# Kernel optimization log

Measured on AMD Instinct MI355X. Metric: run time of the kernel, lower is better.

Reference implementation:

```python
import jax, jax.numpy as jnp
import numpy as np

N_TH1 = 30
LB = 1e-20
UB = 1e20
LB_EXP = -20.0
UB_EXP = 20.0


def make_directions(n_th1):
    # Reproduces the TF __init__ direction sampling on the sphere.
    n_th2 = 2 * (n_th1 - 1) + 1
    th1 = np.linspace(-np.pi / 2, np.pi / 2, n_th1)
    th2 = np.linspace(-np.pi, np.pi, n_th2)
    c1, s1 = np.cos(th1), np.sin(th1)
    c2, s2 = np.cos(th2), np.sin(th2)
    dx = np.outer(c1[1:-1], c2[:-1])          # [n_th1-2, n_th2-1]
    dy = np.outer(c1[1:-1], s2[:-1])
    dz = np.broadcast_to(s1[1:-1, None], dx.shape)
    mid = np.stack([dx, dy, dz], -1).reshape(-1, 3)
    poles = np.array([[c1[0] * c2[0], c1[0] * s2[0], s1[0]],
                      [c1[-1] * c2[0], c1[-1] * s2[0], s1[-1]]])
    return np.concatenate([mid, poles], 0).astype(np.float32)  # [D, 3]


def setup_inputs() -> dict:
    key = jax.random.key(0)
    k1, k2, k3 = jax.random.split(key, 3)
    vertices = jax.random.normal(k1, (8, 64, 32, 3), jnp.float32)
    # smoothness is a p-norm exponent; realistic range [2, 20]
    smoothness = 2.0 + 18.0 * jax.random.uniform(k2, (8, 64), jnp.float32)
    pointcloud = jax.random.normal(k3, (8, 2048, 3), jnp.float32)
    return {"vertices": vertices, "smoothness": smoothness, "pointcloud": pointcloud}


def _spt_forward(vertices, smoothness):
    dirs = jnp.asarray(make_directions(N_TH1))            # [D, 3]
    B, P = vertices.shape[0], vertices.shape[1]
    mean_v = jnp.mean(vertices, axis=2, keepdims=True)    # [B,P,1,3]
    local_v = vertices - mean_v                           # [B,P,V,3]

    # z = <v, x> for every vertex/direction pair -> [B,P,V,D]
    z = jnp.einsum('bpvc,dc->bpvd', local_v, dirs)
    zm = jnp.maximum(z, 0.0)
    p = smoothness[:, :, None, None]                      # [B,P,1,1]

    # dynamic rescaling k = 10^ceil(...) to keep zm^p in fp range
    zm_max = jnp.max(zm, axis=2, keepdims=True)           # [B,P,1,D]
    zm_log = jnp.log(zm_max) / jnp.log(10.0)              # = max over V of log10(zm)
    exponent = zm_log * p
    lk = jnp.where(exponent < LB_EXP, (-15.0 - exponent) / p, 0.0)
    k = 10.0 ** jnp.clip(jnp.ceil(lk), 0.0, UB_EXP)       # [B,P,1,D]
    k = jax.lax.stop_gradient(k)                          # ceil has zero grad anyway

    zm = zm * k
    pos = zm > 0
    # clip(zm^p, lb, ub) - (zm==0)*lb  ==  where(zm>0, clip(zm^p,lb,ub), 0)
    zm_p = jnp.where(pos, jnp.clip(jnp.where(pos, zm, 1.0) ** p, LB, UB), 0.0)
    sum_zm_p = jnp.sum(zm_p, axis=2, keepdims=True)       # [B,P,1,D]
    spos = sum_zm_p > 0
    h = jnp.where(spos, jnp.clip(jnp.where(spos, sum_zm_p, 1.0) ** (1.0 / p), LB, UB), LB)

    # dh/dz = clip((zm/h)^(p-1), lb, ub)
    ratio = zm / h                                        # [B,P,V,D]
    rpos = ratio > 0
    dhdz = jnp.where(rpos, jnp.clip(jnp.where(rpos, ratio, 1.0) ** (p - 1.0), LB, UB), LB)
    # dh/dx = dhdz^T @ vertices -> surface points
    dhdx = jnp.einsum('bpvd,bpvc->bpdc', dhdz, local_v)   # [B,P,D,3]
    surf = dhdx + mean_v                                  # broadcast [B,P,1,3]

    h_out = jnp.clip(h / k, -UB, UB)                      # [B,P,1,D]
    h_out = jnp.transpose(h_out, (0, 1, 3, 2))            # [B,P,D,1]
    local_dirs = jnp.broadcast_to(dirs[None, None], (B, P) + dirs.shape)
    direction_h = jnp.concatenate([local_dirs, h_out], axis=-1)  # [B,P,D,4]
    points = surf.reshape(B, -1, 3)                       # [B, P*D, 3]
    mean_out = mean_v.reshape(B, P, 3)
    return points, direction_h, mean_out, local_v


def reference(vertices, smoothness, pointcloud):
    points, direction_h, mean_out, local_v = _spt_forward(vertices, smoothness)
    B, P = vertices.shape[0], vertices.shape[1]
    # overlap / retraction loops are truncated in the source; placeholders
    overlap = jnp.zeros((B, P, 1), jnp.float32)
    retraction = jnp.zeros((B, P, 1), jnp.float32)
    return (points, direction_h, overlap, retraction, mean_out, local_v)
```

## Files before the change

kernel.cpp:

```cpp
#include <hip/hip_runtime.h>
#include <math.h>

#define NBP 512
#define VV 32
#define DD 1626
#define DHALF 813

#define O_POINTS 0
#define O_DIRH   2497536
#define O_OVER   5827584
#define O_RETR   5828096
#define O_MEAN   5828608
#define O_LOCAL  5830144

#define L10_2 0.3010299956639812f
#define L2_10 3.321928094887362f
#define LH_MIN -66.43856189774725f

__device__ __forceinline__ float fexp2(float x) {
  return __builtin_amdgcn_exp2f(x);
}

__device__ __forceinline__ void make_dir_fast(int d, float& x, float& y, float& z) {
  if (d < 1624) {
    const int i1 = d / 58 + 1;
    const int i2 = d - (i1 - 1) * 58;
    const float STEP = 0.10833078115826873f;
    const float th1 = -1.5707963267948966f + (float)i1 * STEP;
    const float th2 = -3.14159265358979323846f + (float)i2 * STEP;
    const float s1 = __sinf(th1);
    const float c1 = __cosf(th1);
    const float s2 = __sinf(th2);
    const float c2 = __cosf(th2);
    x = c1 * c2; y = c1 * s2; z = s1;
  } else if (d == 1624) {
    x = -6.123234e-17f; y = -7.49880e-33f; z = -1.0f;
  } else {
    x = -6.123234e-17f; y = -7.49880e-33f; z = 1.0f;
  }
}

__global__ __launch_bounds__(256) void spt_kernel(
    const float* __restrict__ vertices,
    const float* __restrict__ smooth,
    float* __restrict__ out)
{
  const int bp   = blockIdx.x;
  const int half = blockIdx.y;
  const int tid  = threadIdx.x;

  const int dbase = half * DHALF;

  float t[VV * 3];
  {
    const float4* vp4 = (const float4*)(vertices + bp * (VV * 3));
#pragma unroll
    for (int j = 0; j < 24; j++) {
      float4 q = vp4[j];
      t[j * 4 + 0] = q.x; t[j * 4 + 1] = q.y;
      t[j * 4 + 2] = q.z; t[j * 4 + 3] = q.w;
    }
  }

  float mxa = 0.f, mxb = 0.f, mya = 0.f, myb = 0.f, mza = 0.f, mzb = 0.f;
#pragma unroll
  for (int i = 0; i < VV; i += 2) {
    mxa += t[3 * i + 0];  mxb += t[3 * i + 3];
    mya += t[3 * i + 1];  myb += t[3 * i + 4];
    mza += t[3 * i + 2];  mzb += t[3 * i + 5];
  }
  const float mx = (mxa + mxb) * (1.0f / 32.0f);
  const float my = (mya + myb) * (1.0f / 32.0f);
  const float mz = (mza + mzb) * (1.0f / 32.0f);

#pragma unroll
  for (int i = 0; i < VV; i++) {
    t[3 * i + 0] -= mx;
    t[3 * i + 1] -= my;
    t[3 * i + 2] -= mz;
  }

  if (half == 1 && tid == 0) {
    float4* lp = (float4*)(out + O_LOCAL + bp * (VV * 3));
#pragma unroll
    for (int j = 0; j < 24; j++) {
      lp[j] = make_float4(t[j * 4 + 0], t[j * 4 + 1], t[j * 4 + 2], t[j * 4 + 3]);
    }
    out[O_MEAN + bp * 3 + 0] = mx;
    out[O_MEAN + bp * 3 + 1] = my;
    out[O_MEAN + bp * 3 + 2] = mz;
    out[O_OVER + bp] = 0.f;
    out[O_RETR + bp] = 0.f;
  }

  const float p     = smooth[bp];
  const float inv_p = 1.0f / p;
  const float pm1   = p - 1.0f;
  const float plt   = p * L10_2;

#pragma unroll 1
  for (int r = 0; r < 4; ++r) {
    const int idx = r * 256 + tid;
    if (idx >= DHALF) break;
    const int d = dbase + idx;
    float dx, dy, dz;
    make_dir_fast(d, dx, dy, dz);

    float zmax = 0.f;
#pragma unroll
    for (int i = 0; i < VV; i++) {
      float zv = fmaxf(fmaf(t[3*i], dx, fmaf(t[3*i+1], dy, t[3*i+2] * dz)), 0.f);
      zmax = fmaxf(zmax, zv);
    }

    const float expo = __log2f(zmax) * plt;
    float kc = 0.f;
    if (expo < -20.f) {
      kc = fminf(fmaxf(ceilf((-15.f - expo) * inv_p), 0.f), 20.f);
    }
    const float kcl = kc * L2_10;
    const float A   = p * kcl;

    float ss0 = 0.f, ss1 = 0.f;
    float ax = 0.f, ay = 0.f, az = 0.f;
#pragma unroll
    for (int i = 0; i < VV; i += 2) {
      float z0 = fmaxf(fmaf(t[3*i+0], dx, fmaf(t[3*i+1], dy, t[3*i+2] * dz)), 0.f);
      float z1 = fmaxf(fmaf(t[3*i+3], dx, fmaf(t[3*i+4], dy, t[3*i+5] * dz)), 0.f);
      float u0 = fexp2(fmaf(pm1, __log2f(z0), A));
      float u1 = fexp2(fmaf(pm1, __log2f(z1), A));
      ss0 = fmaf(u0, z0, ss0);
      ss1 = fmaf(u1, z1, ss1);
      ax = fmaf(u0, t[3*i+0], fmaf(u1, t[3*i+3], ax));
      ay = fmaf(u0, t[3*i+1], fmaf(u1, t[3*i+4], ay));
      az = fmaf(u0, t[3*i+2], fmaf(u1, t[3*i+5], az));
    }
    const float ssum = ss0 + ss1;

    float lh = LH_MIN;
    float C2 = 0.f;
    if (ssum > 0.f) {
      lh = inv_p * __log2f(ssum);
      C2 = fexp2(-fmaf(pm1, lh, kcl));
    }

    const int pbase = bp * DD + d;
    out[O_POINTS + pbase * 3 + 0] = fmaf(C2, ax, mx);
    out[O_POINTS + pbase * 3 + 1] = fmaf(C2, ay, my);
    out[O_POINTS + pbase * 3 + 2] = fmaf(C2, az, mz);

    float4 dvh = make_float4(dx, dy, dz, fexp2(lh - kcl));
    ((float4*)(out + O_DIRH))[pbase] = dvh;
  }
}

extern "C" void kernel_launch(void* const* d_in, const int* in_sizes, int n_in,
                              void* d_out, int out_size, void* d_ws, size_t ws_size,
                              hipStream_t stream) {
  const float* vertices = (const float*)d_in[0];
  const float* smooth   = (const float*)d_in[1];
  float* out = (float*)d_out;

  spt_kernel<<<dim3(NBP, 2), 256, 0, stream>>>(vertices, smooth, out);
}
```

Baseline: 77.39 us.

## Split vertices across thread pairs and fuse max pass with speculative sum

Each direction is now handled by two lanes, each owning 16 of the 32 vertices, with partial sums combined via xor-shuffles. The grid grows to four direction spans per batch-point. The separate zmax pre-pass is folded into the main loop by speculatively assuming no rescaling, and the rare rescaled case is recomputed. Register use per thread drops (launch bounds set to 5 waves) to raise occupancy, at the cost of shuffle traffic, duplicated direction computation per pair and a divergent recompute path when rescaling is needed.

```diff
diff --git a/kernel.cpp b/kernel.cpp
--- a/kernel.cpp
+++ b/kernel.cpp
@@ -4,7 +4,7 @@
 #define NBP 512
 #define VV 32
 #define DD 1626
-#define DHALF 813
+#define DSPAN 407
 
 #define O_POINTS 0
 #define O_DIRH   2497536
@@ -40,57 +40,74 @@
   }
 }
 
-__global__ __launch_bounds__(256) void spt_kernel(
+__global__ __launch_bounds__(256, 5) void spt_kernel(
     const float* __restrict__ vertices,
     const float* __restrict__ smooth,
     float* __restrict__ out)
 {
-  const int bp   = blockIdx.x;
-  const int half = blockIdx.y;
-  const int tid  = threadIdx.x;
+  const int bp  = blockIdx.x;
+  const int bz  = blockIdx.y;
+  const int tid = threadIdx.x;
+  const int sub = tid & 1;
 
-  const int dbase = half * DHALF;
+  const int dbase = bz * DSPAN;
+  const int dend  = (DD - dbase) < DSPAN ? (DD - dbase) : DSPAN;
 
-  float t[VV * 3];
+  float lx[16], ly[16], lz[16];
   {
-    const float4* vp4 = (const float4*)(vertices + bp * (VV * 3));
+    const float4* vp4 = (const float4*)(vertices + bp * (VV * 3) + sub * 48);
+    float tt[48];
 #pragma unroll
-    for (int j = 0; j < 24; j++) {
+    for (int j = 0; j < 12; j++) {
       float4 q = vp4[j];
-      t[j * 4 + 0] = q.x; t[j * 4 + 1] = q.y;
-      t[j * 4 + 2] = q.z; t[j * 4 + 3] = q.w;
+      tt[4 * j + 0] = q.x; tt[4 * j + 1] = q.y;
+      tt[4 * j + 2] = q.z; tt[4 * j + 3] = q.w;
+    }
+#pragma unroll
+    for (int i = 0; i < 16; i++) {
+      lx[i] = tt[3 * i + 0];
+      ly[i] = tt[3 * i + 1];
+      lz[i] = tt[3 * i + 2];
     }
   }
 
-  float mxa = 0.f, mxb = 0.f, mya = 0.f, myb = 0.f, mza = 0.f, mzb = 0.f;
+  float sxa = 0.f, sxb = 0.f, sya = 0.f, syb = 0.f, sza = 0.f, szb = 0.f;
 #pragma unroll
-  for (int i = 0; i < VV; i += 2) {
-    mxa += t[3 * i + 0];  mxb += t[3 * i + 3];
-    mya += t[3 * i + 1];  myb += t[3 * i + 4];
-    mza += t[3 * i + 2];  mzb += t[3 * i + 5];
+  for (int i = 0; i < 16; i += 2) {
+    sxa += lx[i]; sxb += lx[i + 1];
+    sya += ly[i]; syb += ly[i + 1];
+    sza += lz[i]; szb += lz[i + 1];
   }
-  const float mx = (mxa + mxb) * (1.0f / 32.0f);
-  const float my = (mya + myb) * (1.0f / 32.0f);
-  const float mz = (mza + mzb) * (1.0f / 32.0f);
+  float sx = sxa + sxb, sy = sya + syb, sz = sza + szb;
+  sx += __shfl_xor(sx, 1);
+  sy += __shfl_xor(sy, 1);
+  sz += __shfl_xor(sz, 1);
+  const float mx = sx * (1.0f / 32.0f);
+  const float my = sy * (1.0f / 32.0f);
+  const float mz = sz * (1.0f / 32.0f);
 
 #pragma unroll
-  for (int i = 0; i < VV; i++) {
-    t[3 * i + 0] -= mx;
-    t[3 * i + 1] -= my;
-    t[3 * i + 2] -= mz;
+  for (int i = 0; i < 16; i++) {
+    lx[i] -= mx; ly[i] -= my; lz[i] -= mz;
   }
 
-  if (half == 1 && tid == 0) {
-    float4* lp = (float4*)(out + O_LOCAL + bp * (VV * 3));
+  if (bz == 3) {
+    if (tid < 2) {
+      float* lp = out + O_LOCAL + bp * (VV * 3) + sub * 48;
 #pragma unroll
-    for (int j = 0; j < 24; j++) {
-      lp[j] = make_float4(t[j * 4 + 0], t[j * 4 + 1], t[j * 4 + 2], t[j * 4 + 3]);
+      for (int i = 0; i < 16; i++) {
+        lp[3 * i + 0] = lx[i];
+        lp[3 * i + 1] = ly[i];
+        lp[3 * i + 2] = lz[i];
+      }
     }
-    out[O_MEAN + bp * 3 + 0] = mx;
-    out[O_MEAN + bp * 3 + 1] = my;
-    out[O_MEAN + bp * 3 + 2] = mz;
-    out[O_OVER + bp] = 0.f;
-    out[O_RETR + bp] = 0.f;
+    if (tid == 2) {
+      out[O_MEAN + bp * 3 + 0] = mx;
+      out[O_MEAN + bp * 3 + 1] = my;
+      out[O_MEAN + bp * 3 + 2] = mz;
+      out[O_OVER + bp] = 0.f;
+      out[O_RETR + bp] = 0.f;
+    }
   }
 
   const float p     = smooth[bp];
@@ -100,57 +117,70 @@
 
 #pragma unroll 1
   for (int r = 0; r < 4; ++r) {
-    const int idx = r * 256 + tid;
-    if (idx >= DHALF) break;
+    const int idx = r * 128 + (tid >> 1);
+    if (idx >= dend) break;
     const int d = dbase + idx;
     float dx, dy, dz;
     make_dir_fast(d, dx, dy, dz);
 
     float zmax = 0.f;
-#pragma unroll
-    for (int i = 0; i < VV; i++) {
-      float zv = fmaxf(fmaf(t[3*i], dx, fmaf(t[3*i+1], dy, t[3*i+2] * dz)), 0.f);
-      zmax = fmaxf(zmax, zv);
-    }
-
-    const float expo = __log2f(zmax) * plt;
-    float kc = 0.f;
-    if (expo < -20.f) {
-      kc = fminf(fmaxf(ceilf((-15.f - expo) * inv_p), 0.f), 20.f);
-    }
-    const float kcl = kc * L2_10;
-    const float A   = p * kcl;
-
     float ss0 = 0.f, ss1 = 0.f;
     float ax = 0.f, ay = 0.f, az = 0.f;
 #pragma unroll
-    for (int i = 0; i < VV; i += 2) {
-      float z0 = fmaxf(fmaf(t[3*i+0], dx, fmaf(t[3*i+1], dy, t[3*i+2] * dz)), 0.f);
-      float z1 = fmaxf(fmaf(t[3*i+3], dx, fmaf(t[3*i+4], dy, t[3*i+5] * dz)), 0.f);
-      float u0 = fexp2(fmaf(pm1, __log2f(z0), A));
-      float u1 = fexp2(fmaf(pm1, __log2f(z1), A));
+    for (int i = 0; i < 16; i += 2) {
+      float z0 = fmaxf(fmaf(lx[i],     dx, fmaf(ly[i],     dy, lz[i]     * dz)), 0.f);
+      float z1 = fmaxf(fmaf(lx[i + 1], dx, fmaf(ly[i + 1], dy, lz[i + 1] * dz)), 0.f);
+      zmax = fmaxf(zmax, fmaxf(z0, z1));
+      float u0 = fexp2(pm1 * __log2f(z0));
+      float u1 = fexp2(pm1 * __log2f(z1));
       ss0 = fmaf(u0, z0, ss0);
       ss1 = fmaf(u1, z1, ss1);
-      ax = fmaf(u0, t[3*i+0], fmaf(u1, t[3*i+3], ax));
-      ay = fmaf(u0, t[3*i+1], fmaf(u1, t[3*i+4], ay));
-      az = fmaf(u0, t[3*i+2], fmaf(u1, t[3*i+5], az));
+      ax = fmaf(u0, lx[i], fmaf(u1, lx[i + 1], ax));
+      ay = fmaf(u0, ly[i], fmaf(u1, ly[i + 1], ay));
+      az = fmaf(u0, lz[i], fmaf(u1, lz[i + 1], az));
     }
-    const float ssum = ss0 + ss1;
+    zmax = fmaxf(zmax, __shfl_xor(zmax, 1));
+
+    float kcl = 0.f;
+    const float expo = __log2f(zmax) * plt;
+    if (expo < -20.f) {
+      float kc = fminf(fmaxf(ceilf((-15.f - expo) * inv_p), 0.f), 20.f);
+      kcl = kc * L2_10;
+      const float A = p * kcl;
+      ss0 = ss1 = ax = ay = az = 0.f;
+#pragma unroll
+      for (int i = 0; i < 16; i++) {
+        float z0 = fmaxf(fmaf(lx[i], dx, fmaf(ly[i], dy, lz[i] * dz)), 0.f);
+        float u0 = fexp2(fmaf(pm1, __log2f(z0), A));
+        ss0 = fmaf(u0, z0, ss0);
+        ax = fmaf(u0, lx[i], ax);
+        ay = fmaf(u0, ly[i], ay);
+        az = fmaf(u0, lz[i], az);
+      }
+    }
+
+    float ss = ss0 + ss1;
+    ss += __shfl_xor(ss, 1);
+    ax += __shfl_xor(ax, 1);
+    ay += __shfl_xor(ay, 1);
+    az += __shfl_xor(az, 1);
 
     float lh = LH_MIN;
     float C2 = 0.f;
-    if (ssum > 0.f) {
-      lh = inv_p * __log2f(ssum);
+    if (ss > 0.f) {
+      lh = inv_p * __log2f(ss);
       C2 = fexp2(-fmaf(pm1, lh, kcl));
     }
 
     const int pbase = bp * DD + d;
-    out[O_POINTS + pbase * 3 + 0] = fmaf(C2, ax, mx);
-    out[O_POINTS + pbase * 3 + 1] = fmaf(C2, ay, my);
-    out[O_POINTS + pbase * 3 + 2] = fmaf(C2, az, mz);
-
-    float4 dvh = make_float4(dx, dy, dz, fexp2(lh - kcl));
-    ((float4*)(out + O_DIRH))[pbase] = dvh;
+    if (sub == 0) {
+      out[O_POINTS + pbase * 3 + 0] = fmaf(C2, ax, mx);
+      out[O_POINTS + pbase * 3 + 1] = fmaf(C2, ay, my);
+      out[O_POINTS + pbase * 3 + 2] = fmaf(C2, az, mz);
+    } else {
+      float4 dvh = make_float4(dx, dy, dz, fexp2(lh - kcl));
+      ((float4*)(out + O_DIRH))[pbase] = dvh;
+    }
   }
 }
 
@@ -161,5 +191,5 @@
   const float* smooth   = (const float*)d_in[1];
   float* out = (float*)d_out;
 
-  spt_kernel<<<dim3(NBP, 2), 256, 0, stream>>>(vertices, smooth, out);
+  spt_kernel<<<dim3(NBP, 4), 256, 0, stream>>>(vertices, smooth, out);
 }
```

Result: slower. 86.64 us (+12.0%).
